# Kernel optimization log

Measured on AMD Instinct MI355X. Metric: run time of the kernel, lower is better.

## Reference

```python
import jax, jax.numpy as jnp
import numpy as np


def _seg(data, ids, n):
    return jax.ops.segment_sum(data, ids, num_segments=n)


def _cheb_lap_weights(src, dst, ew, n):
    # PyG ChebConv norm: L = I - D^-1/2 A D^-1/2, scaled L_hat = 2L/lambda_max - I.
    # With default lambda_max=2.0 the diagonal of L_hat is 0 and off-diagonal is -norm.
    deg = _seg(ew, src, n)
    dinv = jnp.where(deg > 0, deg ** -0.5, 0.0)
    return -(dinv[src] * ew * dinv[dst])  # [E]


def _cheb_apply(x, w_lap, src, dst, n, W, b):
    # Chebyshev recursion: Tx0=x, Tx1=L x, Tx_k = 2 L Tx_{k-1} - Tx_{k-2}
    def L(v):
        return _seg(w_lap[:, None] * v[src], dst, n)
    Tx0 = x
    Tx1 = L(x)
    out = Tx0 @ W[0] + Tx1 @ W[1]
    for k in range(2, W.shape[0]):
        Tx2 = 2.0 * L(Tx1) - Tx0
        out = out + Tx2 @ W[k]
        Tx0, Tx1 = Tx1, Tx2
    return out + b


def _gcn(x, src, dst, ew, n, W, b):
    # PyG GCNConv: add self-loops (weight 1), sym norm D~^-1/2 (A+I) D~^-1/2, x@W first.
    deg = _seg(ew, dst, n) + 1.0
    dinv = jnp.where(deg > 0, deg ** -0.5, 0.0)
    xw = x @ W
    norm = dinv[src] * ew * dinv[dst]
    out = _seg(norm[:, None] * xw[src], dst, n) + (dinv * dinv)[:, None] * xw
    return out + b


def setup_inputs() -> dict:
    key = jax.random.key(0)
    ks = jax.random.split(key, 16)
    num_nodes, B, T = 64, 256, 64
    hid, out_ch, ncls = 64, 64, 4
    epg = num_nodes * 16  # edges per graph (avg degree 16)
    N = num_nodes * B
    E = epg * B
    off = (jnp.arange(B, dtype=jnp.int64) * num_nodes)[:, None]
    src = (jax.random.randint(ks[0], (B, epg), 0, num_nodes) + off).reshape(-1)
    dst = (jax.random.randint(ks[1], (B, epg), 0, num_nodes) + off).reshape(-1)
    return {
        "x": jax.random.normal(ks[2], (N, T), jnp.float32),
        "edge_weight": jax.random.uniform(ks[3], (E,), jnp.float32, 0.1, 1.0),
        "wA": jax.random.normal(ks[4], (4, 1, hid), jnp.float32) * 0.1,
        "bA": jax.random.normal(ks[5], (hid,), jnp.float32) * 0.1,
        "wB": jax.random.normal(ks[6], (4, hid, hid), jnp.float32) * 0.1,
        "bB": jax.random.normal(ks[7], (hid,), jnp.float32) * 0.1,
        "w1": jax.random.normal(ks[8], (hid, out_ch), jnp.float32) * 0.1,
        "b1": jax.random.normal(ks[9], (out_ch,), jnp.float32) * 0.1,
        "w2": jax.random.normal(ks[10], (out_ch, out_ch // 2), jnp.float32) * 0.1,
        "b2": jax.random.normal(ks[11], (out_ch // 2,), jnp.float32) * 0.1,
        "wfc": jax.random.normal(ks[12], (num_nodes * out_ch // 2, ncls), jnp.float32) * 0.1,
        "bfc": jax.random.normal(ks[13], (ncls,), jnp.float32) * 0.1,
        "edge_src": src.astype(jnp.int64),
        "edge_dst": dst.astype(jnp.int64),
        "num_nodes": 64,
    }


def reference(x, edge_weight, wA, bA, wB, bB, w1, b1, w2, b2, wfc, bfc, edge_src, edge_dst, num_nodes):
    N = x.shape[0]
    B = N // num_nodes
    w_lap = _cheb_lap_weights(edge_src, edge_dst, edge_weight, N)

    def step(h, xt):  # xt: [N]
        a = _cheb_apply(xt[:, None], w_lap, edge_src, edge_dst, N, wA, bA)
        bh = _cheb_apply(h, w_lap, edge_src, edge_dst, N, wB, bB)
        h_new = jax.nn.sigmoid(a + bh)
        return h_new, None

    h0 = jnp.zeros((N, wB.shape[1]), x.dtype)
    h, _ = jax.lax.scan(step, h0, x.T)  # loop over T; only last h is used downstream

    z = jax.nn.relu(_gcn(h, edge_src, edge_dst, edge_weight, N, w1, b1))
    z = jax.nn.relu(_gcn(z, edge_src, edge_dst, edge_weight, N, w2, b2))
    z = z.reshape(B, -1)  # [B, num_nodes * out_ch/2]
    return jax.nn.log_softmax(z @ wfc + bfc, axis=1)
```

## Files before the change

### kernel.cpp

```cpp
#include <hip/hip_runtime.h>
#include <math.h>

#define NODES 64
#define NSTEPS 64
#define EPG 1024
#define NTHREADS 1024
#define NBLOCKS 256

typedef _Float16 f16;
typedef f16 f16x8 __attribute__((ext_vector_type(8)));
typedef f16 f16x4 __attribute__((ext_vector_type(4)));
typedef float f32x4 __attribute__((ext_vector_type(4)));

#define OFF_Y1    0
#define OFF_Y2    9216
#define OFF_Y3    18432
#define OFF_HA    27648
#define OFF_HB    36864
#define OFF_TT    46080
#define OFF_ZT    55296
#define OFF_WT    88064
#define OFF_DEG   126976
#define OFF_DINV  127232
#define OFF_BSUM  127488
#define OFF_LOGIT 127744
#define SMEM_BYTES 127872

__device__ __forceinline__ f32x4 mfma16(f16x8 a, f16x8 b, f32x4 c) {
  return __builtin_amdgcn_mfma_f32_16x16x32_f16(a, b, c, 0, 0, 0);
}

__device__ __forceinline__ f32x4 mm64t(const f16* __restrict__ A, const f16* __restrict__ B,
                                       int rb, int cb, int lrow, int lk)
{
  f32x4 d = (f32x4){0.f, 0.f, 0.f, 0.f};
#pragma unroll
  for (int ch = 0; ch < 2; ++ch) {
    const f16x8 a = *(const f16x8*)(A + (rb * 16 + lrow) * 72 + ch * 32 + lk * 8);
    const f16x8 b = *(const f16x8*)(B + (cb * 16 + lrow) * 72 + ch * 32 + lk * 8);
    d = mfma16(a, b, d);
  }
  return d;
}

template<int K>
__device__ __forceinline__ void mm4x4_acc(float acc[4][4],
                                          const float* __restrict__ A, int lda, int arow,
                                          const float* __restrict__ Bm, int ldb, int j4)
{
#pragma unroll 2
  for (int kc = 0; kc < K; kc += 4) {
    float av[4][4];
    float bv[4][4];
#pragma unroll
    for (int rr = 0; rr < 4; ++rr) {
      const float4 t = *(const float4*)(A + (arow + rr) * lda + kc);
      av[rr][0] = t.x; av[rr][1] = t.y; av[rr][2] = t.z; av[rr][3] = t.w;
    }
#pragma unroll
    for (int kk = 0; kk < 4; ++kk) {
      const float4 t = *(const float4*)(Bm + (kc + kk) * ldb + j4);
      bv[kk][0] = t.x; bv[kk][1] = t.y; bv[kk][2] = t.z; bv[kk][3] = t.w;
    }
#pragma unroll
    for (int rr = 0; rr < 4; ++rr)
#pragma unroll
      for (int cc = 0; cc < 4; ++cc) {
        float s = acc[rr][cc];
#pragma unroll
        for (int kk = 0; kk < 4; ++kk) s += av[rr][kk] * bv[kk][cc];
        acc[rr][cc] = s;
      }
  }
}

__global__ __launch_bounds__(NTHREADS)
void gcrnn_mfma3(const float* __restrict__ x,
                 const float* __restrict__ ew,
                 const float* __restrict__ wA,
                 const float* __restrict__ bA,
                 const float* __restrict__ wB,
                 const float* __restrict__ bB,
                 const float* __restrict__ w1,
                 const float* __restrict__ b1,
                 const float* __restrict__ w2,
                 const float* __restrict__ b2,
                 const float* __restrict__ wfc,
                 const float* __restrict__ bfc,
                 const int* __restrict__ esrc,
                 const int* __restrict__ edst,
                 float* __restrict__ out)
{
  __shared__ __align__(16) char smem[SMEM_BYTES];

  f16*   sM1   = (f16*)(smem + OFF_Y1);
  f16*   sM2   = (f16*)(smem + OFF_Y2);
  f16*   sM3   = (f16*)(smem + OFF_Y3);
  f16*   sHA   = (f16*)(smem + OFF_HA);
  f16*   sHB   = (f16*)(smem + OFF_HB);
  f16*   sTt   = (f16*)(smem + OFF_TT);
  f16*   sZt   = (f16*)(smem + OFF_ZT);
  float* sLgF  = (float*)(smem + OFF_ZT);
  f16*   sWt   = (f16*)(smem + OFF_WT);
  float* sDeg  = (float*)(smem + OFF_DEG);
  float* sDinv = (float*)(smem + OFF_DINV);
  float* sBsum = (float*)(smem + OFF_BSUM);
  float* sLogit= (float*)(smem + OFF_LOGIT);

  const int b = blockIdx.x, tid = threadIdx.x;
  const int gbase = b * NODES, ebase = b * EPG;
  const int wid = tid >> 6, lane = tid & 63;
  const int lrow = lane & 15, lk = lane >> 4;

  const int rbS = wid >> 2, cbS = wid & 3;
  const int fbA = wid >> 2;
  const int cbB = wid >> 2, nbB = wid & 3;

  for (int idx = tid; idx < 4096; idx += NTHREADS) sLgF[idx] = 0.f;
  if (tid < 64) { sDeg[tid] = 0.f; sBsum[tid] = bA[tid] + bB[tid]; }
  for (int idx = tid; idx < 64 * 260; idx += NTHREADS) {
    const int k = idx >> 6, c = idx & 63;
    const float v = (k < 256) ? wB[(k >> 6) * 4096 + (k & 63) * 64 + c]
                              : wA[(k - 256) * 64 + c];
    sWt[c * 304 + k] = (f16)v;
  }
  for (int idx = tid; idx < 64 * 44; idx += NTHREADS) {
    const int c = idx / 44, j = idx - c * 44;
    sWt[c * 304 + 260 + j] = (f16)0.f;
  }
  for (int idx = tid; idx < 4096; idx += NTHREADS) {
    const int n = idx >> 6, t = idx & 63;
    sTt[t * 72 + n] = (f16)x[gbase * 64 + idx];
  }
  __syncthreads();

  for (int e = tid; e < EPG; e += NTHREADS)
    atomicAdd(&sDeg[esrc[ebase + e] - gbase], ew[ebase + e]);
  __syncthreads();
  if (tid < 64) { const float d = sDeg[tid]; sDinv[tid] = (d > 0.f) ? rsqrtf(d) : 0.f; }
  __syncthreads();
  for (int e = tid; e < EPG; e += NTHREADS) {
    const int sl = esrc[ebase + e] - gbase, dl = edst[ebase + e] - gbase;
    atomicAdd(&sLgF[dl * 64 + sl], -(sDinv[sl] * ew[ebase + e] * sDinv[dl]));
  }
  __syncthreads();
  for (int idx = tid; idx < 4096; idx += NTHREADS) {
    const int i = idx >> 6, j = idx & 63;
    const f16 v = (f16)sLgF[idx];
    sM1[i * 72 + j] = v;
    sHA[j * 72 + i] = v;
  }
  __syncthreads();

  {
    f32x4 d;
    d = mm64t(sHA, sM1, rbS, cbS, lrow, lk);
    {
      const int p0 = rbS * 16 + lk * 4, q = cbS * 16 + lrow;
      f16x4 w;
#pragma unroll
      for (int r = 0; r < 4; ++r) w[r] = (f16)(2.f * d[r] - ((p0 + r) == q ? 1.f : 0.f));
      *(f16x4*)(sM2 + q * 72 + p0) = w;
    }
    d = mm64t(sM1, sHA, rbS, cbS, lrow, lk);
    {
      const int p0 = rbS * 16 + lk * 4, q = cbS * 16 + lrow;
      f16x4 w;
#pragma unroll
      for (int r = 0; r < 4; ++r) w[r] = (f16)(2.f * d[r] - ((p0 + r) == q ? 1.f : 0.f));
      *(f16x4*)(sHB + q * 72 + p0) = w;
    }
    d = mm64t(sM1, sTt, rbS, cbS, lrow, lk);
    {
      const int p0 = rbS * 16 + lk * 4, q = cbS * 16 + lrow;
#pragma unroll
      for (int r = 0; r < 4; ++r) sZt[q * 256 + (p0 + r) * 4 + 1] = (f16)d[r];
    }
    for (int idx = tid; idx < 4096; idx += NTHREADS) {
      const int t = idx >> 6, n = idx & 63;
      sZt[t * 256 + n * 4 + 0] = sTt[t * 72 + n];
    }
  }
  __syncthreads();

  {
    f32x4 d;
    d = mm64t(sHB, sM1, rbS, cbS, lrow, lk);
    {
      const int p0 = rbS * 16 + lk * 4, q = cbS * 16 + lrow;
      const f16x4 lv = *(const f16x4*)(sM1 + q * 72 + p0);
      f16x4 w;
#pragma unroll
      for (int r = 0; r < 4; ++r) w[r] = (f16)(2.f * d[r] - (float)lv[r]);
      *(f16x4*)(sM3 + q * 72 + p0) = w;
    }
    d = mm64t(sM2, sTt, rbS, cbS, lrow, lk);
    {
      const int p0 = rbS * 16 + lk * 4, q = cbS * 16 + lrow;
#pragma unroll
      for (int r = 0; r < 4; ++r) sZt[q * 256 + (p0 + r) * 4 + 2] = (f16)d[r];
    }
  }
  __syncthreads();

  {
    f32x4 d = mm64t(sM3, sTt, rbS, cbS, lrow, lk);
    const int p0 = rbS * 16 + lk * 4, q = cbS * 16 + lrow;
#pragma unroll
    for (int r = 0; r < 4; ++r) sZt[q * 256 + (p0 + r) * 4 + 3] = (f16)d[r];
  }
  __syncthreads();

  f16x8 mfrag[3][2];
  int   mnb[3];
  f16*  mYb[3];
  f16x8 wfrag[9];
  f32x4 bsr;
  {
#pragma unroll
    for (int i = 0; i < 3; ++i) {
      const int tau = 3 * wid + i;
      const int k = (tau % 12) >> 2;
      const int nb = tau & 3;
      mnb[i] = nb;
      mYb[i] = (f16*)smem + k * 4608;
#pragma unroll
      for (int ch = 0; ch < 2; ++ch)
        mfrag[i][ch] = *(const f16x8*)(mYb[i] + (nb * 16 + lrow) * 72 + ch * 32 + lk * 8);
    }
#pragma unroll
    for (int ch = 0; ch < 9; ++ch)
      wfrag[ch] = *(const f16x8*)(sWt + (cbB * 16 + lrow) * 304 + ch * 32 + lk * 8);
#pragma unroll
    for (int r = 0; r < 4; ++r) bsr[r] = sBsum[cbB * 16 + lk * 4 + r];
    for (int idx = tid; idx < 3 * 2304; idx += NTHREADS)
      ((int*)(smem + OFF_HA))[idx] = 0;
  }
  __syncthreads();

  const int bn = nbB * 16 + lrow;

  auto step = [&](int t, const f16* __restrict__ hrCur, f16* __restrict__ hrNxt) {
    {
      const f16x8 a0 = *(const f16x8*)(sTt + (fbA * 16 + lrow) * 72 + lk * 8);
      const f16x8 a1 = *(const f16x8*)(sTt + (fbA * 16 + lrow) * 72 + 32 + lk * 8);
      f32x4 y0 = (f32x4){0.f,0.f,0.f,0.f}, y1 = y0, y2 = y0;
      y0 = mfma16(a0, mfrag[0][0], y0);
      y1 = mfma16(a0, mfrag[1][0], y1);
      y2 = mfma16(a0, mfrag[2][0], y2);
      y0 = mfma16(a1, mfrag[0][1], y0);
      y1 = mfma16(a1, mfrag[1][1], y1);
      y2 = mfma16(a1, mfrag[2][1], y2);
      f32x4 yy[3] = {y0, y1, y2};
#pragma unroll
      for (int i = 0; i < 3; ++i) {
        f16x4 w;
#pragma unroll
        for (int r = 0; r < 4; ++r) w[r] = (f16)yy[i][r];
        *(f16x4*)(mYb[i] + (mnb[i] * 16 + lrow) * 72 + fbA * 16 + lk * 4) = w;
      }
    }
    __syncthreads();
    {
      f32x4 pa = bsr;
      f32x4 pb = (f32x4){0.f, 0.f, 0.f, 0.f};
      f16x8 bb;
      bb = *(const f16x8*)(hrCur + bn * 72 + lk * 8);       pa = mfma16(wfrag[0], bb, pa);
      bb = *(const f16x8*)(hrCur + bn * 72 + 32 + lk * 8);  pb = mfma16(wfrag[1], bb, pb);
      bb = *(const f16x8*)(sM1 + bn * 72 + lk * 8);         pa = mfma16(wfrag[2], bb, pa);
      bb = *(const f16x8*)(sM1 + bn * 72 + 32 + lk * 8);    pb = mfma16(wfrag[3], bb, pb);
      bb = *(const f16x8*)(sM2 + bn * 72 + lk * 8);         pa = mfma16(wfrag[4], bb, pa);
      bb = *(const f16x8*)(sM2 + bn * 72 + 32 + lk * 8);    pb = mfma16(wfrag[5], bb, pb);
      bb = *(const f16x8*)(sM3 + bn * 72 + lk * 8);         pa = mfma16(wfrag[6], bb, pa);
      bb = *(const f16x8*)(sM3 + bn * 72 + 32 + lk * 8);    pb = mfma16(wfrag[7], bb, pb);
      {
        const f16x4 zv = *(const f16x4*)(sZt + t * 256 + bn * 4);
        f16x8 zb;
        zb[0] = zv[0]; zb[1] = zv[1]; zb[2] = zv[2]; zb[3] = zv[3];
        zb[4] = (f16)0.f; zb[5] = (f16)0.f; zb[6] = (f16)0.f; zb[7] = (f16)0.f;
        pa = mfma16(wfrag[8], zb, pa);
      }
      const f32x4 p = pa + pb;
      f16x4 hv;
      float hf[4];
#pragma unroll
      for (int r = 0; r < 4; ++r) {
        hf[r] = 1.f / (1.f + __expf(-p[r]));
        hv[r] = (f16)hf[r];
      }
      *(f16x4*)(hrNxt + bn * 72 + cbB * 16 + lk * 4) = hv;
#pragma unroll
      for (int r = 0; r < 4; ++r)
        sTt[(cbB * 16 + lk * 4 + r) * 72 + bn] = hv[r];
    }
    __syncthreads();
  };

#pragma unroll 1
  for (int tt = 0; tt < NSTEPS / 2; ++tt) {
    step(2 * tt, sHA, sHB);
    step(2 * tt + 1, sHB, sHA);
  }

  float* sLgG = (float*)(smem + OFF_ZT);
  float* sT1g = (float*)(smem + OFF_WT);
  float* sT2g = (float*)(smem + OFF_WT + 17408);

  for (int idx = tid; idx < 64 * 68; idx += NTHREADS) sLgG[idx] = 0.f;
  if (tid < 64) sDeg[tid] = 0.f;
  for (int idx = tid; idx < 4096; idx += NTHREADS) {
    const int n = idx >> 6, c = idx & 63;
    sT1g[n * 68 + c] = (float)sHA[n * 72 + c];
  }
  if (tid < 4) sLogit[tid] = bfc[tid];
  __syncthreads();
  for (int e = tid; e < EPG; e += NTHREADS)
    atomicAdd(&sDeg[edst[ebase + e] - gbase], ew[ebase + e]);
  __syncthreads();
  if (tid < 64) sDinv[tid] = rsqrtf(sDeg[tid] + 1.f);
  __syncthreads();
  for (int e = tid; e < EPG; e += NTHREADS) {
    const int sl = esrc[ebase + e] - gbase, dl = edst[ebase + e] - gbase;
    atomicAdd(&sLgG[dl * 68 + sl], sDinv[sl] * ew[ebase + e] * sDinv[dl]);
  }
  __syncthreads();
  if (tid < 64) sLgG[tid * 68 + tid] += sDinv[tid] * sDinv[tid];
  __syncthreads();

  const bool isTile = tid < 256;
  const int i4 = ((tid >> 4) & 15) * 4;
  const int j4 = (tid & 15) * 4;

  if (isTile) {
    float m[4][4] = {};
    mm4x4_acc<64>(m, sT1g, 68, i4, w1, 64, j4);
#pragma unroll
    for (int rr = 0; rr < 4; ++rr)
      *(float4*)(sT2g + (i4 + rr) * 68 + j4) = make_float4(m[rr][0], m[rr][1], m[rr][2], m[rr][3]);
  }
  __syncthreads();
  if (isTile) {
    float m[4][4] = {};
    mm4x4_acc<64>(m, sLgG, 68, i4, sT2g, 68, j4);
#pragma unroll
    for (int rr = 0; rr < 4; ++rr) {
      float4 o;
      o.x = fmaxf(m[rr][0] + b1[j4 + 0], 0.f);
      o.y = fmaxf(m[rr][1] + b1[j4 + 1], 0.f);
      o.z = fmaxf(m[rr][2] + b1[j4 + 2], 0.f);
      o.w = fmaxf(m[rr][3] + b1[j4 + 3], 0.f);
      *(float4*)(sT1g + (i4 + rr) * 68 + j4) = o;
    }
  }
  __syncthreads();
  if (isTile && j4 < 32) {
    float m[4][4] = {};
    mm4x4_acc<64>(m, sT1g, 68, i4, w2, 32, j4);
#pragma unroll
    for (int rr = 0; rr < 4; ++rr)
      *(float4*)(sT2g + (i4 + rr) * 68 + j4) = make_float4(m[rr][0], m[rr][1], m[rr][2], m[rr][3]);
  }
  __syncthreads();
  if (isTile && j4 < 32) {
    float m[4][4] = {};
    mm4x4_acc<64>(m, sLgG, 68, i4, sT2g, 68, j4);
#pragma unroll
    for (int rr = 0; rr < 4; ++rr) {
      float4 o;
      o.x = fmaxf(m[rr][0] + b2[j4 + 0], 0.f);
      o.y = fmaxf(m[rr][1] + b2[j4 + 1], 0.f);
      o.z = fmaxf(m[rr][2] + b2[j4 + 2], 0.f);
      o.w = fmaxf(m[rr][3] + b2[j4 + 3], 0.f);
      *(float4*)(sT1g + (i4 + rr) * 68 + j4) = o;
    }
  }
  __syncthreads();

  float p0 = 0.f, p1 = 0.f, p2 = 0.f, p3 = 0.f;
  for (int f = tid; f < 2048; f += NTHREADS) {
    const int n = f >> 5, c = f & 31;
    const float v = sT1g[n * 68 + c];
    const float4 wv = *(const float4*)(wfc + f * 4);
    p0 += v * wv.x; p1 += v * wv.y; p2 += v * wv.z; p3 += v * wv.w;
  }
#pragma unroll
  for (int off = 1; off < 64; off <<= 1) {
    p0 += __shfl_xor(p0, off);
    p1 += __shfl_xor(p1, off);
    p2 += __shfl_xor(p2, off);
    p3 += __shfl_xor(p3, off);
  }
  if ((tid & 63) == 0) {
    atomicAdd(&sLogit[0], p0);
    atomicAdd(&sLogit[1], p1);
    atomicAdd(&sLogit[2], p2);
    atomicAdd(&sLogit[3], p3);
  }
  __syncthreads();
  if (tid == 0) {
    const float l0 = sLogit[0], l1 = sLogit[1], l2 = sLogit[2], l3 = sLogit[3];
    const float mx = fmaxf(fmaxf(l0, l1), fmaxf(l2, l3));
    const float s = expf(l0 - mx) + expf(l1 - mx) + expf(l2 - mx) + expf(l3 - mx);
    const float lse = mx + logf(s);
    out[b * 4 + 0] = l0 - lse;
    out[b * 4 + 1] = l1 - lse;
    out[b * 4 + 2] = l2 - lse;
    out[b * 4 + 3] = l3 - lse;
  }
}

extern "C" void kernel_launch(void* const* d_in, const int* in_sizes, int n_in,
                              void* d_out, int out_size, void* d_ws, size_t ws_size,
                              hipStream_t stream) {
  gcrnn_mfma3<<<NBLOCKS, NTHREADS, 0, stream>>>(
      (const float*)d_in[0],
      (const float*)d_in[1],
      (const float*)d_in[2],
      (const float*)d_in[3],
      (const float*)d_in[4],
      (const float*)d_in[5],
      (const float*)d_in[6],
      (const float*)d_in[7],
      (const float*)d_in[8],
      (const float*)d_in[9],
      (const float*)d_in[10],
      (const float*)d_in[11],
      (const int*)d_in[12],
      (const int*)d_in[13],
      (float*)d_out);
}
```

Measured before the change: 112.0 us.

## Split recurrence into specialised A/B waves with register-resident fragments and swizzled layouts

```diff
diff --git a/kernel.cpp b/kernel.cpp
--- a/kernel.cpp
+++ b/kernel.cpp
@@ -4,7 +4,7 @@
 #define NODES 64
 #define NSTEPS 64
 #define EPG 1024
-#define NTHREADS 1024
+#define NTHREADS 512
 #define NBLOCKS 256
 
 typedef _Float16 f16;
@@ -12,23 +12,36 @@
 typedef f16 f16x4 __attribute__((ext_vector_type(4)));
 typedef float f32x4 __attribute__((ext_vector_type(4)));
 
-#define OFF_Y1    0
-#define OFF_Y2    9216
-#define OFF_Y3    18432
-#define OFF_HA    27648
-#define OFF_HB    36864
-#define OFF_TT    46080
+#define OFF_M1    0
+#define OFF_YF    0
+#define OFF_M2    9216
+#define OFF_M3    18432
+#define OFF_M1T   27648
+#define OFF_HF    27648
+#define OFF_M2T   36864
+#define OFF_HTF   36864
+#define OFF_XT    46080
 #define OFF_ZT    55296
 #define OFF_WT    88064
-#define OFF_DEG   126976
-#define OFF_DINV  127232
-#define OFF_BSUM  127488
-#define OFF_LOGIT 127744
-#define SMEM_BYTES 127872
+#define OFF_LGF   126976
+#define OFF_DEG   143360
+#define OFF_DINV  143616
+#define OFF_BSUM  143872
+#define OFF_LOGIT 144128
+#define SMEM_BYTES 144384
 
 __device__ __forceinline__ f32x4 mfma16(f16x8 a, f16x8 b, f32x4 c) {
   return __builtin_amdgcn_mfma_f32_16x16x32_f16(a, b, c, 0, 0, 0);
 }
+
+#if __has_builtin(__builtin_amdgcn_mfma_f32_16x16x16f16)
+#define HAVE_MFMA_K16 1
+__device__ __forceinline__ f32x4 mfma16k16(f16x4 a, f16x4 b, f32x4 c) {
+  return __builtin_amdgcn_mfma_f32_16x16x16f16(a, b, c, 0, 0, 0);
+}
+#else
+#define HAVE_MFMA_K16 0
+#endif
 
 __device__ __forceinline__ f32x4 mm64t(const f16* __restrict__ A, const f16* __restrict__ B,
                                        int rb, int cb, int lrow, int lk)
@@ -74,8 +87,8 @@
   }
 }
 
-__global__ __launch_bounds__(NTHREADS)
-void gcrnn_mfma3(const float* __restrict__ x,
+__global__ __launch_bounds__(NTHREADS, 2)
+void gcrnn_mfma4(const float* __restrict__ x,
                  const float* __restrict__ ew,
                  const float* __restrict__ wA,
                  const float* __restrict__ bA,
@@ -93,15 +106,15 @@
 {
   __shared__ __align__(16) char smem[SMEM_BYTES];
 
-  f16*   sM1   = (f16*)(smem + OFF_Y1);
-  f16*   sM2   = (f16*)(smem + OFF_Y2);
-  f16*   sM3   = (f16*)(smem + OFF_Y3);
-  f16*   sHA   = (f16*)(smem + OFF_HA);
-  f16*   sHB   = (f16*)(smem + OFF_HB);
-  f16*   sTt   = (f16*)(smem + OFF_TT);
+  f16*   sM1   = (f16*)(smem + OFF_M1);
+  f16*   sM2   = (f16*)(smem + OFF_M2);
+  f16*   sM3   = (f16*)(smem + OFF_M3);
+  f16*   sM1T  = (f16*)(smem + OFF_M1T);
+  f16*   sM2T  = (f16*)(smem + OFF_M2T);
+  f16*   sXT   = (f16*)(smem + OFF_XT);
   f16*   sZt   = (f16*)(smem + OFF_ZT);
-  float* sLgF  = (float*)(smem + OFF_ZT);
   f16*   sWt   = (f16*)(smem + OFF_WT);
+  float* sLgF  = (float*)(smem + OFF_LGF);
   float* sDeg  = (float*)(smem + OFF_DEG);
   float* sDinv = (float*)(smem + OFF_DINV);
   float* sBsum = (float*)(smem + OFF_BSUM);
@@ -111,10 +124,9 @@
   const int gbase = b * NODES, ebase = b * EPG;
   const int wid = tid >> 6, lane = tid & 63;
   const int lrow = lane & 15, lk = lane >> 4;
-
-  const int rbS = wid >> 2, cbS = wid & 3;
-  const int fbA = wid >> 2;
-  const int cbB = wid >> 2, nbB = wid & 3;
+  const bool isA = wid < 4;
+  const int fb = wid;
+  const int nb = wid & 3;
 
   for (int idx = tid; idx < 4096; idx += NTHREADS) sLgF[idx] = 0.f;
   if (tid < 64) { sDeg[tid] = 0.f; sBsum[tid] = bA[tid] + bB[tid]; }
@@ -130,7 +142,7 @@
   }
   for (int idx = tid; idx < 4096; idx += NTHREADS) {
     const int n = idx >> 6, t = idx & 63;
-    sTt[t * 72 + n] = (f16)x[gbase * 64 + idx];
+    sXT[t * 72 + n] = (f16)x[gbase * 64 + idx];
   }
   __syncthreads();
 
@@ -148,13 +160,17 @@
     const int i = idx >> 6, j = idx & 63;
     const f16 v = (f16)sLgF[idx];
     sM1[i * 72 + j] = v;
-    sHA[j * 72 + i] = v;
-  }
-  __syncthreads();
-
-  {
+    sM1T[j * 72 + i] = v;
+  }
+  __syncthreads();
+
+  const int rbS = wid >> 1;
+
+#pragma unroll
+  for (int s = 0; s < 2; ++s) {
+    const int cbS = (wid & 1) * 2 + s;
     f32x4 d;
-    d = mm64t(sHA, sM1, rbS, cbS, lrow, lk);
+    d = mm64t(sM1T, sM1, rbS, cbS, lrow, lk);
     {
       const int p0 = rbS * 16 + lk * 4, q = cbS * 16 + lrow;
       f16x4 w;
@@ -162,30 +178,32 @@
       for (int r = 0; r < 4; ++r) w[r] = (f16)(2.f * d[r] - ((p0 + r) == q ? 1.f : 0.f));
       *(f16x4*)(sM2 + q * 72 + p0) = w;
     }
-    d = mm64t(sM1, sHA, rbS, cbS, lrow, lk);
+    d = mm64t(sM1, sM1T, rbS, cbS, lrow, lk);
     {
       const int p0 = rbS * 16 + lk * 4, q = cbS * 16 + lrow;
       f16x4 w;
 #pragma unroll
       for (int r = 0; r < 4; ++r) w[r] = (f16)(2.f * d[r] - ((p0 + r) == q ? 1.f : 0.f));
-      *(f16x4*)(sHB + q * 72 + p0) = w;
-    }
-    d = mm64t(sM1, sTt, rbS, cbS, lrow, lk);
+      *(f16x4*)(sM2T + q * 72 + p0) = w;
+    }
+    d = mm64t(sM1, sXT, rbS, cbS, lrow, lk);
     {
       const int p0 = rbS * 16 + lk * 4, q = cbS * 16 + lrow;
 #pragma unroll
       for (int r = 0; r < 4; ++r) sZt[q * 256 + (p0 + r) * 4 + 1] = (f16)d[r];
     }
-    for (int idx = tid; idx < 4096; idx += NTHREADS) {
-      const int t = idx >> 6, n = idx & 63;
-      sZt[t * 256 + n * 4 + 0] = sTt[t * 72 + n];
-    }
-  }
-  __syncthreads();
-
-  {
+  }
+  for (int idx = tid; idx < 4096; idx += NTHREADS) {
+    const int t = idx >> 6, n = idx & 63;
+    sZt[t * 256 + n * 4 + 0] = sXT[t * 72 + n];
+  }
+  __syncthreads();
+
+#pragma unroll
+  for (int s = 0; s < 2; ++s) {
+    const int cbS = (wid & 1) * 2 + s;
     f32x4 d;
-    d = mm64t(sHB, sM1, rbS, cbS, lrow, lk);
+    d = mm64t(sM2T, sM1, rbS, cbS, lrow, lk);
     {
       const int p0 = rbS * 16 + lk * 4, q = cbS * 16 + lrow;
       const f16x4 lv = *(const f16x4*)(sM1 + q * 72 + p0);
@@ -194,7 +212,7 @@
       for (int r = 0; r < 4; ++r) w[r] = (f16)(2.f * d[r] - (float)lv[r]);
       *(f16x4*)(sM3 + q * 72 + p0) = w;
     }
-    d = mm64t(sM2, sTt, rbS, cbS, lrow, lk);
+    d = mm64t(sM2, sXT, rbS, cbS, lrow, lk);
     {
       const int p0 = rbS * 16 + lk * 4, q = cbS * 16 + lrow;
 #pragma unroll
@@ -203,114 +221,129 @@
   }
   __syncthreads();
 
-  {
-    f32x4 d = mm64t(sM3, sTt, rbS, cbS, lrow, lk);
+#pragma unroll
+  for (int s = 0; s < 2; ++s) {
+    const int cbS = (wid & 1) * 2 + s;
+    f32x4 d = mm64t(sM3, sXT, rbS, cbS, lrow, lk);
     const int p0 = rbS * 16 + lk * 4, q = cbS * 16 + lrow;
 #pragma unroll
     for (int r = 0; r < 4; ++r) sZt[q * 256 + (p0 + r) * 4 + 3] = (f16)d[r];
   }
   __syncthreads();
 
-  f16x8 mfrag[3][2];
-  int   mnb[3];
-  f16*  mYb[3];
-  f16x8 wfrag[9];
-  f32x4 bsr;
-  {
-#pragma unroll
-    for (int i = 0; i < 3; ++i) {
-      const int tau = 3 * wid + i;
-      const int k = (tau % 12) >> 2;
-      const int nb = tau & 3;
-      mnb[i] = nb;
-      mYb[i] = (f16*)smem + k * 4608;
-#pragma unroll
-      for (int ch = 0; ch < 2; ++ch)
-        mfrag[i][ch] = *(const f16x8*)(mYb[i] + (nb * 16 + lrow) * 72 + ch * 32 + lk * 8);
-    }
-#pragma unroll
-    for (int ch = 0; ch < 9; ++ch)
-      wfrag[ch] = *(const f16x8*)(sWt + (cbB * 16 + lrow) * 304 + ch * 32 + lk * 8);
-#pragma unroll
-    for (int r = 0; r < 4; ++r) bsr[r] = sBsum[cbB * 16 + lk * 4 + r];
-    for (int idx = tid; idx < 3 * 2304; idx += NTHREADS)
-      ((int*)(smem + OFF_HA))[idx] = 0;
-  }
-  __syncthreads();
-
-  const int bn = nbB * 16 + lrow;
-
-  auto step = [&](int t, const f16* __restrict__ hrCur, f16* __restrict__ hrNxt) {
-    {
-      const f16x8 a0 = *(const f16x8*)(sTt + (fbA * 16 + lrow) * 72 + lk * 8);
-      const f16x8 a1 = *(const f16x8*)(sTt + (fbA * 16 + lrow) * 72 + 32 + lk * 8);
-      f32x4 y0 = (f32x4){0.f,0.f,0.f,0.f}, y1 = y0, y2 = y0;
-      y0 = mfma16(a0, mfrag[0][0], y0);
-      y1 = mfma16(a0, mfrag[1][0], y1);
-      y2 = mfma16(a0, mfrag[2][0], y2);
-      y0 = mfma16(a1, mfrag[0][1], y0);
-      y1 = mfma16(a1, mfrag[1][1], y1);
-      y2 = mfma16(a1, mfrag[2][1], y2);
-      f32x4 yy[3] = {y0, y1, y2};
-#pragma unroll
-      for (int i = 0; i < 3; ++i) {
-        f16x4 w;
-#pragma unroll
-        for (int r = 0; r < 4; ++r) w[r] = (f16)yy[i][r];
-        *(f16x4*)(mYb[i] + (mnb[i] * 16 + lrow) * 72 + fbA * 16 + lk * 4) = w;
+  f16x8 frag[36];
+  float bsrv[4];
+  f16x4 iF;
+#pragma unroll
+  for (int e = 0; e < 4; ++e) iF[e] = (f16)((lrow == lk * 4 + e) ? 1.f : 0.f);
+
+  if (isA) {
+#pragma unroll
+    for (int k = 0; k < 3; ++k)
+#pragma unroll
+      for (int nn = 0; nn < 4; ++nn)
+#pragma unroll
+        for (int ch = 0; ch < 2; ++ch)
+          frag[(k * 4 + nn) * 2 + ch] =
+            *(const f16x8*)((const f16*)(smem + OFF_M1 + k * 9216) + (nn * 16 + lrow) * 72 + ch * 32 + lk * 8);
+  } else {
+#pragma unroll
+    for (int cb = 0; cb < 4; ++cb) {
+#pragma unroll
+      for (int j = 0; j < 9; ++j)
+        frag[cb * 9 + j] = *(const f16x8*)(sWt + (cb * 16 + lrow) * 304 + j * 32 + lk * 8);
+      bsrv[cb] = sBsum[cb * 16 + lrow];
+    }
+  }
+  for (int idx = tid; idx < 2048; idx += NTHREADS) {
+    ((int*)(smem + OFF_HF))[idx] = 0;
+    ((int*)(smem + OFF_HTF))[idx] = 0;
+  }
+  __syncthreads();
+
+#pragma unroll 1
+  for (int t = 0; t < NSTEPS; ++t) {
+    f32x4 p0v, p1v, p2v, p3v;
+    if (isA) {
+      const f16x8 aT0 = *(const f16x8*)(smem + OFF_HTF + (fb * 2 + 0) * 1024 + lane * 16);
+      const f16x8 aT1 = *(const f16x8*)(smem + OFF_HTF + (fb * 2 + 1) * 1024 + lane * 16);
+      const int lslot = (lrow + 16 * ((fb & 1) * 2 + (lk >> 1))) * 16 + (lk & 1) * 8;
+#pragma unroll
+      for (int k = 0; k < 3; ++k)
+#pragma unroll
+        for (int nn = 0; nn < 4; ++nn) {
+          f32x4 d = (f32x4){0.f, 0.f, 0.f, 0.f};
+          d = mfma16(aT0, frag[(k * 4 + nn) * 2 + 0], d);
+          d = mfma16(aT1, frag[(k * 4 + nn) * 2 + 1], d);
+          f16x4 w;
+#pragma unroll
+          for (int r = 0; r < 4; ++r) w[r] = (f16)d[r];
+          *(f16x4*)(smem + OFF_YF + (((k * 4 + nn) * 2 + (fb >> 1)) * 1024) + lslot) = w;
+        }
+    } else {
+      const f16x8 ah0 = *(const f16x8*)(smem + OFF_HF + (nb * 2 + 0) * 1024 + lane * 16);
+      const f16x8 ah1 = *(const f16x8*)(smem + OFF_HF + (nb * 2 + 1) * 1024 + lane * 16);
+      const f16x4 zv = *(const f16x4*)(smem + OFF_ZT + t * 512 + (nb * 16 + lrow) * 8);
+      f16x8 az;
+      az[0] = zv[0]; az[1] = zv[1]; az[2] = zv[2]; az[3] = zv[3];
+      az[4] = (f16)0.f; az[5] = (f16)0.f; az[6] = (f16)0.f; az[7] = (f16)0.f;
+      p0v = (f32x4){bsrv[0], bsrv[0], bsrv[0], bsrv[0]};
+      p1v = (f32x4){bsrv[1], bsrv[1], bsrv[1], bsrv[1]};
+      p2v = (f32x4){bsrv[2], bsrv[2], bsrv[2], bsrv[2]};
+      p3v = (f32x4){bsrv[3], bsrv[3], bsrv[3], bsrv[3]};
+      p0v = mfma16(ah0, frag[0 * 9 + 0], p0v); p0v = mfma16(ah1, frag[0 * 9 + 1], p0v); p0v = mfma16(az, frag[0 * 9 + 8], p0v);
+      p1v = mfma16(ah0, frag[1 * 9 + 0], p1v); p1v = mfma16(ah1, frag[1 * 9 + 1], p1v); p1v = mfma16(az, frag[1 * 9 + 8], p1v);
+      p2v = mfma16(ah0, frag[2 * 9 + 0], p2v); p2v = mfma16(ah1, frag[2 * 9 + 1], p2v); p2v = mfma16(az, frag[2 * 9 + 8], p2v);
+      p3v = mfma16(ah0, frag[3 * 9 + 0], p3v); p3v = mfma16(ah1, frag[3 * 9 + 1], p3v); p3v = mfma16(az, frag[3 * 9 + 8], p3v);
+    }
+    __syncthreads();
+
+    if (!isA) {
+#pragma unroll
+      for (int k = 0; k < 3; ++k)
+#pragma unroll
+        for (int ch = 0; ch < 2; ++ch) {
+          const f16x8 ay = *(const f16x8*)(smem + OFF_YF + (((k * 4 + nb) * 2 + ch) * 1024) + lane * 16);
+          const int j = 2 + 2 * k + ch;
+          p0v = mfma16(ay, frag[0 * 9 + j], p0v);
+          p1v = mfma16(ay, frag[1 * 9 + j], p1v);
+          p2v = mfma16(ay, frag[2 * 9 + j], p2v);
+          p3v = mfma16(ay, frag[3 * 9 + j], p3v);
+        }
+#pragma unroll
+      for (int cb = 0; cb < 4; ++cb) {
+        const f32x4 pv = (cb == 0) ? p0v : (cb == 1) ? p1v : (cb == 2) ? p2v : p3v;
+        f16x4 hv;
+#pragma unroll
+        for (int r = 0; r < 4; ++r) hv[r] = (f16)(1.f / (1.f + __expf(-pv[r])));
+        *(f16x4*)(smem + OFF_HTF + ((cb * 2 + (nb >> 1)) * 64 + lrow + 16 * ((nb & 1) * 2 + (lk >> 1))) * 16 + (lk & 1) * 8) = hv;
+#if HAVE_MFMA_K16
+        f32x4 d2 = mfma16k16(hv, iF, (f32x4){0.f, 0.f, 0.f, 0.f});
+        f16x4 h2;
+#pragma unroll
+        for (int r = 0; r < 4; ++r) h2[r] = (f16)d2[r];
+        *(f16x4*)(smem + OFF_HF + ((nb * 2 + (cb >> 1)) * 64 + lrow + 16 * ((cb & 1) * 2 + (lk >> 1))) * 16 + (lk & 1) * 8) = h2;
+#else
+#pragma unroll
+        for (int r = 0; r < 4; ++r)
+          ((f16*)(smem + OFF_HF))[((nb * 2 + (cb >> 1)) * 64 + (lk * 4 + r) + 16 * ((cb & 1) * 2 + (lrow >> 3))) * 8 + (lrow & 7)] = hv[r];
+#endif
       }
     }
     __syncthreads();
-    {
-      f32x4 pa = bsr;
-      f32x4 pb = (f32x4){0.f, 0.f, 0.f, 0.f};
-      f16x8 bb;
-      bb = *(const f16x8*)(hrCur + bn * 72 + lk * 8);       pa = mfma16(wfrag[0], bb, pa);
-      bb = *(const f16x8*)(hrCur + bn * 72 + 32 + lk * 8);  pb = mfma16(wfrag[1], bb, pb);
-      bb = *(const f16x8*)(sM1 + bn * 72 + lk * 8);         pa = mfma16(wfrag[2], bb, pa);
-      bb = *(const f16x8*)(sM1 + bn * 72 + 32 + lk * 8);    pb = mfma16(wfrag[3], bb, pb);
-      bb = *(const f16x8*)(sM2 + bn * 72 + lk * 8);         pa = mfma16(wfrag[4], bb, pa);
-      bb = *(const f16x8*)(sM2 + bn * 72 + 32 + lk * 8);    pb = mfma16(wfrag[5], bb, pb);
-      bb = *(const f16x8*)(sM3 + bn * 72 + lk * 8);         pa = mfma16(wfrag[6], bb, pa);
-      bb = *(const f16x8*)(sM3 + bn * 72 + 32 + lk * 8);    pb = mfma16(wfrag[7], bb, pb);
-      {
-        const f16x4 zv = *(const f16x4*)(sZt + t * 256 + bn * 4);
-        f16x8 zb;
-        zb[0] = zv[0]; zb[1] = zv[1]; zb[2] = zv[2]; zb[3] = zv[3];
-        zb[4] = (f16)0.f; zb[5] = (f16)0.f; zb[6] = (f16)0.f; zb[7] = (f16)0.f;
-        pa = mfma16(wfrag[8], zb, pa);
-      }
-      const f32x4 p = pa + pb;
-      f16x4 hv;
-      float hf[4];
-#pragma unroll
-      for (int r = 0; r < 4; ++r) {
-        hf[r] = 1.f / (1.f + __expf(-p[r]));
-        hv[r] = (f16)hf[r];
-      }
-      *(f16x4*)(hrNxt + bn * 72 + cbB * 16 + lk * 4) = hv;
-#pragma unroll
-      for (int r = 0; r < 4; ++r)
-        sTt[(cbB * 16 + lk * 4 + r) * 72 + bn] = hv[r];
-    }
-    __syncthreads();
-  };
-
-#pragma unroll 1
-  for (int tt = 0; tt < NSTEPS / 2; ++tt) {
-    step(2 * tt, sHA, sHB);
-    step(2 * tt + 1, sHB, sHA);
   }
 
   float* sLgG = (float*)(smem + OFF_ZT);
   float* sT1g = (float*)(smem + OFF_WT);
   float* sT2g = (float*)(smem + OFF_WT + 17408);
+  const f16* hF = (const f16*)(smem + OFF_HF);
 
   for (int idx = tid; idx < 64 * 68; idx += NTHREADS) sLgG[idx] = 0.f;
   if (tid < 64) sDeg[tid] = 0.f;
   for (int idx = tid; idx < 4096; idx += NTHREADS) {
     const int n = idx >> 6, c = idx & 63;
-    sT1g[n * 68 + c] = (float)sHA[n * 72 + c];
+    const f16 v = hF[(((n >> 4) * 2 + (c >> 5)) * 64 + (n & 15) + 16 * ((c >> 3) & 3)) * 8 + (c & 7)];
+    sT1g[n * 68 + c] = (float)v;
   }
   if (tid < 4) sLogit[tid] = bfc[tid];
   __syncthreads();
@@ -376,25 +409,25 @@
   }
   __syncthreads();
 
-  float p0 = 0.f, p1 = 0.f, p2 = 0.f, p3 = 0.f;
+  float q0 = 0.f, q1 = 0.f, q2 = 0.f, q3 = 0.f;
   for (int f = tid; f < 2048; f += NTHREADS) {
     const int n = f >> 5, c = f & 31;
     const float v = sT1g[n * 68 + c];
     const float4 wv = *(const float4*)(wfc + f * 4);
-    p0 += v * wv.x; p1 += v * wv.y; p2 += v * wv.z; p3 += v * wv.w;
+    q0 += v * wv.x; q1 += v * wv.y; q2 += v * wv.z; q3 += v * wv.w;
   }
 #pragma unroll
   for (int off = 1; off < 64; off <<= 1) {
-    p0 += __shfl_xor(p0, off);
-    p1 += __shfl_xor(p1, off);
-    p2 += __shfl_xor(p2, off);
-    p3 += __shfl_xor(p3, off);
+    q0 += __shfl_xor(q0, off);
+    q1 += __shfl_xor(q1, off);
+    q2 += __shfl_xor(q2, off);
+    q3 += __shfl_xor(q3, off);
   }
   if ((tid & 63) == 0) {
-    atomicAdd(&sLogit[0], p0);
-    atomicAdd(&sLogit[1], p1);
-    atomicAdd(&sLogit[2], p2);
-    atomicAdd(&sLogit[3], p3);
+    atomicAdd(&sLogit[0], q0);
+    atomicAdd(&sLogit[1], q1);
+    atomicAdd(&sLogit[2], q2);
+    atomicAdd(&sLogit[3], q3);
   }
   __syncthreads();
   if (tid == 0) {
@@ -412,7 +445,7 @@
 extern "C" void kernel_launch(void* const* d_in, const int* in_sizes, int n_in,
                               void* d_out, int out_size, void* d_ws, size_t ws_size,
                               hipStream_t stream) {
-  gcrnn_mfma3<<<NBLOCKS, NTHREADS, 0, stream>>>(
+  gcrnn_mfma4<<<NBLOCKS, NTHREADS, 0, stream>>>(
       (const float*)d_in[0],
       (const float*)d_in[1],
       (const float*)d_in[2],
```

Result: no change. 111.8 us (-0.2%).
